# Optimization experiments

Hardware: AMD Instinct MI355X
Metric: run time of the kernel (lower is better)

The kernel has to match this reference:

```python
import jax, jax.numpy as jnp
import numpy as np

N_NODES = 100000
N_EDGES = 1600000
N_GRAPHS = 128


def setup_inputs() -> dict:
    key = jax.random.key(0)
    ks = jax.random.split(key, 8)
    x = jax.random.normal(ks[0], (N_NODES, 384), dtype=jnp.float32)
    edge_index = jax.random.randint(ks[1], (2, N_EDGES), 0, N_NODES, dtype=jnp.int64)
    batch = jnp.sort(jax.random.randint(ks[2], (N_NODES,), 0, N_GRAPHS, dtype=jnp.int64))
    W1 = jax.random.normal(ks[3], (384, 128), dtype=jnp.float32) * (1.0 / np.sqrt(384))
    b1 = jnp.zeros((128,), dtype=jnp.float32)
    W2 = jax.random.normal(ks[4], (128, 64), dtype=jnp.float32) * (1.0 / np.sqrt(128))
    b2 = jnp.zeros((64,), dtype=jnp.float32)
    Wlin = jax.random.normal(ks[5], (64, 2), dtype=jnp.float32) * (1.0 / np.sqrt(64))
    blin = jnp.zeros((2,), dtype=jnp.float32)
    return {"x": x, "edge_index": edge_index, "batch": batch,
            "W1": W1, "b1": b1, "W2": W2, "b2": b2, "Wlin": Wlin, "blin": blin}


def gcn_conv(x, src, dst, W, b, n_nodes):
    # PyG GCNConv: self-loops + symmetric normalization D^{-1/2} A_hat D^{-1/2},
    # linear transform first (out_dim < in_dim -> cheaper messages).
    h = x @ W  # [N, out]
    deg = jax.ops.segment_sum(jnp.ones_like(dst, dtype=h.dtype), dst,
                              num_segments=n_nodes) + 1.0  # self-loop weight
    dis = jax.lax.rsqrt(deg)  # deg >= 1 always (self-loop)
    norm = dis[src] * dis[dst]  # per-edge normalization [E]
    msg = h[src] * norm[:, None]  # gather + scale [E, out]
    agg = jax.ops.segment_sum(msg, dst, num_segments=n_nodes)
    agg = agg + h * (dis * dis)[:, None]  # self-loop contribution
    return agg + b


def reference(x, edge_index, batch, W1, b1, W2, b2, Wlin, blin):
    src, dst = edge_index[0], edge_index[1]
    n_nodes = x.shape[0]
    h = jax.nn.relu(gcn_conv(x, src, dst, W1, b1, n_nodes))
    h = jax.nn.relu(gcn_conv(h, src, dst, W2, b2, n_nodes))
    # global_mean_pool over graph ids
    sums = jax.ops.segment_sum(h, batch, num_segments=N_GRAPHS)
    cnts = jax.ops.segment_sum(jnp.ones((n_nodes,), dtype=h.dtype), batch,
                               num_segments=N_GRAPHS)
    pooled = sums / jnp.maximum(cnts, 1.0)[:, None]  # [G, 64]
    # dropout is identity in eval mode
    return pooled @ Wlin + blin  # [G, 2]
```

## Files before the change

kernel.cpp:

```cpp
#include <hip/hip_runtime.h>


#define NN 100000
#define NG 128
#define BNODES 256
#define NBUK ((NN + BNODES - 1) / BNODES)
#define BCAP 6144

typedef __attribute__((ext_vector_type(8))) short short8;
typedef __attribute__((ext_vector_type(8))) unsigned short u16x8;
typedef __attribute__((ext_vector_type(4))) float f32x4;

__device__ __forceinline__ unsigned short f2bf(float f) {
    union { float f; unsigned u; } v; v.f = f;
    unsigned r = v.u + 0x7fffu + ((v.u >> 16) & 1u);
    return (unsigned short)(r >> 16);
}
__device__ __forceinline__ float bf2f(unsigned short h) {
    union { unsigned u; float f; } v; v.u = ((unsigned)h) << 16;
    return v.f;
}

__device__ __forceinline__ void gload_lds16(const float* g, void* l) {
    __builtin_amdgcn_global_load_lds(
        (const __attribute__((address_space(1))) void*)g,
        (__attribute__((address_space(3))) void*)l, 16, 0, 0);
}

__global__ __launch_bounds__(256) void init_kernel(int* __restrict__ bcnt,
                                                   float* __restrict__ pooled,
                                                   float* __restrict__ cnt) {
    const int i = blockIdx.x * 256 + threadIdx.x;
    if (i < NBUK) bcnt[i] = 0;
    if (i < NG * 64) pooled[i] = 0.f;
    if (i < NG) cnt[i] = 0.f;
}

__global__ __launch_bounds__(256) void bucket_scatter(const int* __restrict__ src,
                                                      const int* __restrict__ dst,
                                                      int* __restrict__ bcnt,
                                                      int2* __restrict__ pairs, int E) {
    __shared__ int hist[NBUK];
    __shared__ int lbase[NBUK];
    __shared__ int lfill[NBUK];
    const int t = threadIdx.x;
    const int chunk = (E + gridDim.x - 1) / gridDim.x;
    const int lo = blockIdx.x * chunk;
    const int hi = min(E, lo + chunk);
    for (int b = t; b < NBUK; b += 256) { hist[b] = 0; lfill[b] = 0; }
    __syncthreads();
    for (int i = lo + t; i < hi; i += 256)
        atomicAdd(&hist[dst[i] >> 8], 1);
    __syncthreads();
    for (int b = t; b < NBUK; b += 256)
        lbase[b] = hist[b] ? atomicAdd(&bcnt[b], hist[b]) : 0;
    __syncthreads();
    for (int i = lo + t; i < hi; i += 256) {
        const int s = src[i], d = dst[i];
        const int b = d >> 8;
        const int off = atomicAdd(&lfill[b], 1);
        pairs[(size_t)b * BCAP + lbase[b] + off] = make_int2(s, d);
    }
}

__global__ __launch_bounds__(512) void bucket_scan(const int* __restrict__ bcnt,
                                                   int* __restrict__ bbase,
                                                   int* __restrict__ rowptr,
                                                   int N, int E) {
    __shared__ int sm[512];
    const int t = threadIdx.x;
    sm[t] = (t < NBUK) ? bcnt[t] : 0;
    __syncthreads();
    for (int d = 1; d < 512; d <<= 1) {
        int a = (t >= d) ? sm[t - d] : 0;
        __syncthreads();
        sm[t] += a;
        __syncthreads();
    }
    if (t <= NBUK) bbase[t] = (t == 0) ? 0 : sm[t - 1];
    if (t == 0) rowptr[N] = E;
}

__global__ __launch_bounds__(256) void bucket_build(const int2* __restrict__ pairs,
                                                    const int* __restrict__ bcnt,
                                                    const int* __restrict__ bbase,
                                                    int* __restrict__ rowptr,
                                                    float* __restrict__ dis,
                                                    int* __restrict__ col, int N) {
    __shared__ int cnt[BNODES];
    __shared__ int sm[BNODES];
    __shared__ int pref[BNODES];
    __shared__ int fillc[BNODES];
    const int b = blockIdx.x;
    const int t = threadIdx.x;
    const int nbase = b * BNODES;
    const int ecnt = bcnt[b];
    const int2* ep = pairs + (size_t)b * BCAP;
    const int gbase = bbase[b];

    cnt[t] = 0;
    fillc[t] = 0;
    __syncthreads();
    for (int i = t; i < ecnt; i += 256)
        atomicAdd(&cnt[ep[i].y & (BNODES - 1)], 1);
    __syncthreads();
    sm[t] = cnt[t];
    __syncthreads();
    for (int d = 1; d < 256; d <<= 1) {
        int a = (t >= d) ? sm[t - d] : 0;
        __syncthreads();
        sm[t] += a;
        __syncthreads();
    }
    pref[t] = sm[t] - cnt[t];
    const int node = nbase + t;
    if (node < N) {
        rowptr[node] = gbase + pref[t];
        dis[node] = rsqrtf((float)cnt[t] + 1.0f);
    }
    __syncthreads();
    for (int i = t; i < ecnt; i += 256) {
        const int2 e = ep[i];
        const int d = e.y & (BNODES - 1);
        const int pos = gbase + pref[d] + atomicAdd(&fillc[d], 1);
        col[pos] = e.x;
    }
}

__global__ __launch_bounds__(256) void pack_w(const float* __restrict__ W,
                                              unsigned short* __restrict__ packH,
                                              unsigned short* __restrict__ packL,
                                              int K, int BN) {
    const int idx = blockIdx.x * blockDim.x + threadIdx.x;
    if (idx >= K * BN) return;
    const int e = idx & 7;
    const int l = (idx >> 3) & 63;
    const int rest = idx >> 9;
    const int NF = BN >> 4;
    const int nf = rest % NF;
    const int ks = rest / NF;
    const int n = nf * 16 + (l & 15);
    const int k = ks * 32 + ((l >> 4) & 3) * 8 + e;
    const float v = W[(size_t)k * BN + n];
    const unsigned short h = f2bf(v);
    packH[idx] = h;
    packL[idx] = f2bf(v - bf2f(h));
}

template <int BN, int K>
__global__ __launch_bounds__(256) void gemm_mfma(const float* __restrict__ A,
                                                 const unsigned short* __restrict__ WpH,
                                                 const unsigned short* __restrict__ WpL,
                                                 const float* __restrict__ scale,
                                                 unsigned short* __restrict__ Out,
                                                 int N) {
    constexpr int BM = 64;
    constexpr int NK = K / 32;
    constexpr int WROWS = (BN == 128) ? 2 : 4;
    constexpr int WCOLS = (BN == 128) ? 2 : 1;
    constexpr int WTM = BM / WROWS;
    constexpr int MF = WTM / 16;
    constexpr int NFW = (BN / WCOLS) / 16;
    constexpr int NFB = BN / 16;

    __shared__ float AsF[2][4][16][32];

    const int t = threadIdx.x;
    const int wid = t >> 6, lane = t & 63;
    const int wr = wid / WCOLS, wc = wid % WCOLS;
    const int r0 = blockIdx.x * BM;

    const int dmarow0 = min(r0 + wid * 16 + (lane >> 3), NN - 1);
    const int dmarow1 = min(r0 + wid * 16 + 8 + (lane >> 3), NN - 1);
    const float* dmap0 = A + (size_t)dmarow0 * K + (lane & 7) * 4;
    const float* dmap1 = A + (size_t)dmarow1 * K + (lane & 7) * 4;

    auto stageA = [&](int buf, int ks) {
        gload_lds16(dmap0 + ks * 32, &AsF[buf][wid][0][0]);
        gload_lds16(dmap1 + ks * 32, &AsF[buf][wid][8][0]);
    };
    auto loadB = [&](int ks, short8* bH, short8* bL) {
#pragma unroll
        for (int n = 0; n < NFW; ++n) {
            const int nfg = wc * NFW + n;
            const int base = ((ks * NFB + nfg) * 64 + lane) * 8;
            bH[n] = *(const short8*)&WpH[base];
            bL[n] = *(const short8*)&WpL[base];
        }
    };

    f32x4 acc[MF][NFW];
#pragma unroll
    for (int m = 0; m < MF; ++m)
#pragma unroll
        for (int n = 0; n < NFW; ++n) acc[m][n] = (f32x4){0.f, 0.f, 0.f, 0.f};

    stageA(0, 0);
    short8 bHc[NFW], bLc[NFW];
    loadB(0, bHc, bLc);

#pragma unroll
    for (int ks = 0; ks < NK; ++ks) {
        const int cur = ks & 1;
        __syncthreads();
        short8 bHn[NFW], bLn[NFW];
        if (ks + 1 < NK) {
            stageA(cur ^ 1, ks + 1);
            loadB(ks + 1, bHn, bLn);
        }
#pragma unroll
        for (int m = 0; m < MF; ++m) {
            const int mf = wr * MF + m;
            const float* fp = &AsF[cur][mf][lane & 15][(lane >> 4) * 8];
            const f32x4 f0 = *(const f32x4*)fp;
            const f32x4 f1 = *(const f32x4*)(fp + 4);
            short8 aH;
            aH[0] = (short)f2bf(f0[0]);
            aH[1] = (short)f2bf(f0[1]);
            aH[2] = (short)f2bf(f0[2]);
            aH[3] = (short)f2bf(f0[3]);
            aH[4] = (short)f2bf(f1[0]);
            aH[5] = (short)f2bf(f1[1]);
            aH[6] = (short)f2bf(f1[2]);
            aH[7] = (short)f2bf(f1[3]);
#pragma unroll
            for (int n = 0; n < NFW; ++n) {
                acc[m][n] = __builtin_amdgcn_mfma_f32_16x16x32_bf16(aH, bHc[n], acc[m][n], 0, 0, 0);
                acc[m][n] = __builtin_amdgcn_mfma_f32_16x16x32_bf16(aH, bLc[n], acc[m][n], 0, 0, 0);
            }
        }
        if (ks + 1 < NK) {
#pragma unroll
            for (int n = 0; n < NFW; ++n) {
                bHc[n] = bHn[n];
                bLc[n] = bLn[n];
            }
        }
    }

#pragma unroll
    for (int m = 0; m < MF; ++m) {
        const int row0 = r0 + wr * WTM + m * 16 + ((lane >> 4) << 2);
        float sc[4];
#pragma unroll
        for (int r = 0; r < 4; ++r) sc[r] = (row0 + r < N) ? scale[row0 + r] : 0.f;
#pragma unroll
        for (int n = 0; n < NFW; ++n) {
            const int cn = wc * (NFW * 16) + n * 16 + (lane & 15);
#pragma unroll
            for (int r = 0; r < 4; ++r) {
                if (row0 + r < N)
                    Out[(size_t)(row0 + r) * BN + cn] = f2bf(acc[m][n][r] * sc[r]);
            }
        }
    }
}

template <int COLS>
__global__ __launch_bounds__(256) void agg_gather(const int* __restrict__ rowptr,
                                                  const int* __restrict__ col,
                                                  const float* __restrict__ dis,
                                                  const unsigned short* __restrict__ Hs,
                                                  const float* __restrict__ bias,
                                                  float* __restrict__ Out, int N) {
    constexpr int NPW = (COLS == 128) ? 1 : 2;
    constexpr int LPN = 64 / NPW;
    constexpr int LPR = COLS / 8;
    constexpr int NSG = LPN / LPR;
    const int gw = (int)((blockIdx.x * blockDim.x + threadIdx.x) >> 6);
    const int lane = threadIdx.x & 63;
    const int sub = lane / LPN;
    const int nl = lane % LPN;
    const int esub = nl / LPR;
    const int sl = nl % LPR;
    const int node = gw * NPW + sub;
    const int lgbase = sub * LPN;

    float acc[8];
#pragma unroll
    for (int k = 0; k < 8; ++k) acc[k] = 0.f;

    int base = 0, len = 0;
    const int nodec = (node < N) ? node : 0;
    if (node < N) {
        base = rowptr[node];
        len = rowptr[node + 1] - base;
    }

    for (int j0 = 0; j0 < len; j0 += LPN) {
        const int remain = min(LPN, len - j0);
        const int sidx = (nl < remain) ? col[base + j0 + nl] : nodec;
        const int qtr = (remain + NSG - 1) / NSG;
        const int off = esub * qtr;
        int u = 0;
        for (; u + 8 <= qtr; u += 8) {
            u16x8 hv[8];
            float wv[8];
#pragma unroll
            for (int b = 0; b < 8; ++b) {
                const int idx = off + u + b;
                const int s = __shfl(sidx, lgbase + idx);
                wv[b] = (idx < remain) ? 1.f : 0.f;
                hv[b] = *(const u16x8*)(Hs + (size_t)s * COLS + sl * 8);
            }
#pragma unroll
            for (int b = 0; b < 8; ++b)
#pragma unroll
                for (int k = 0; k < 8; ++k)
                    acc[k] = fmaf(bf2f(hv[b][k]), wv[b], acc[k]);
        }
        for (; u + 4 <= qtr; u += 4) {
            u16x8 hv[4];
            float wv[4];
#pragma unroll
            for (int b = 0; b < 4; ++b) {
                const int idx = off + u + b;
                const int s = __shfl(sidx, lgbase + idx);
                wv[b] = (idx < remain) ? 1.f : 0.f;
                hv[b] = *(const u16x8*)(Hs + (size_t)s * COLS + sl * 8);
            }
#pragma unroll
            for (int b = 0; b < 4; ++b)
#pragma unroll
                for (int k = 0; k < 8; ++k)
                    acc[k] = fmaf(bf2f(hv[b][k]), wv[b], acc[k]);
        }
        for (; u < qtr; ++u) {
            const int idx = off + u;
            const int s = __shfl(sidx, lgbase + idx);
            const float w = (idx < remain) ? 1.f : 0.f;
            const u16x8 hv = *(const u16x8*)(Hs + (size_t)s * COLS + sl * 8);
#pragma unroll
            for (int k = 0; k < 8; ++k)
                acc[k] = fmaf(bf2f(hv[k]), w, acc[k]);
        }
    }

#pragma unroll
    for (int k = 0; k < 8; ++k) {
        acc[k] += __shfl_xor(acc[k], LPR);
        acc[k] += __shfl_xor(acc[k], 2 * LPR);
    }

    if (node < N && esub == 0) {
        const float dd = dis[node];
        const u16x8 hsb = *(const u16x8*)(Hs + (size_t)node * COLS + sl * 8);
        const f32x4 bv0 = *(const f32x4*)(bias + sl * 8);
        const f32x4 bv1 = *(const f32x4*)(bias + sl * 8 + 4);
        f32x4 o0, o1;
#pragma unroll
        for (int k = 0; k < 4; ++k) {
            o0[k] = fmaxf(fmaf(acc[k] + bf2f(hsb[k]), dd, bv0[k]), 0.f);
            o1[k] = fmaxf(fmaf(acc[k + 4] + bf2f(hsb[k + 4]), dd, bv1[k]), 0.f);
        }
        *(f32x4*)(Out + (size_t)node * COLS + sl * 8) = o0;
        *(f32x4*)(Out + (size_t)node * COLS + sl * 8 + 4) = o1;
    }
}

__global__ __launch_bounds__(256) void pool_kernel(const float* __restrict__ H,
                                                   const int* __restrict__ batch,
                                                   float* __restrict__ pooled,
                                                   float* __restrict__ cnt, int N) {
    const int c = threadIdx.x & 63;
    const int w = threadIdx.x >> 6;
    const int row0 = blockIdx.x * 128 + w * 32;
    if (row0 >= N) return;
    const int nr = min(32, N - row0);

    float v[32];
    int b[32];
#pragma unroll
    for (int i = 0; i < 32; ++i) {
        const int r = row0 + i;
        if (i < nr) {
            v[i] = H[(size_t)r * 64 + c];
            b[i] = batch[r];
        } else {
            v[i] = 0.f;
            b[i] = -1;
        }
    }
    int cur = b[0];
    float sum = 0.f, csum = 0.f;
#pragma unroll
    for (int i = 0; i < 32; ++i) {
        if (i < nr) {
            if (b[i] != cur) {
                atomicAdd(&pooled[cur * 64 + c], sum);
                if (c == 0) atomicAdd(&cnt[cur], csum);
                cur = b[i];
                sum = 0.f;
                csum = 0.f;
            }
            sum += v[i];
            csum += 1.f;
        }
    }
    atomicAdd(&pooled[cur * 64 + c], sum);
    if (c == 0) atomicAdd(&cnt[cur], csum);
}

__global__ __launch_bounds__(256) void final_kernel(const float* __restrict__ pooled,
                                                    const float* __restrict__ cnt,
                                                    const float* __restrict__ Wlin,
                                                    const float* __restrict__ blin,
                                                    float* __restrict__ out) {
    const int t = threadIdx.x;
    const int g = t >> 1, o = t & 1;
    const float inv = 1.0f / fmaxf(cnt[g], 1.0f);
    float s = 0.f;
#pragma unroll
    for (int j = 0; j < 64; ++j) s = fmaf(pooled[g * 64 + j], Wlin[j * 2 + o], s);
    out[t] = s * inv + blin[o];
}

extern "C" void kernel_launch(void* const* d_in, const int* in_sizes, int n_in,
                              void* d_out, int out_size, void* d_ws, size_t ws_size,
                              hipStream_t stream) {
    const float* x     = (const float*)d_in[0];
    const int*   edge  = (const int*)d_in[1];
    const int*   batch = (const int*)d_in[2];
    const float* W1    = (const float*)d_in[3];
    const float* b1    = (const float*)d_in[4];
    const float* W2    = (const float*)d_in[5];
    const float* b2    = (const float*)d_in[6];
    const float* Wlin  = (const float*)d_in[7];
    const float* blin  = (const float*)d_in[8];
    float* out = (float*)d_out;

    const int N = NN;
    const int E = in_sizes[1] / 2;
    const int* src = edge;
    const int* dst = edge + E;

    char* ws = (char*)d_ws;
    size_t off = 0;
    auto alloc = [&](size_t bytes) -> void* {
        void* p = ws + off;
        off += (bytes + 511) & ~(size_t)511;
        return p;
    };
    float* dis    = (float*)alloc((size_t)N * 4);
    int*   rowptr = (int*)alloc((size_t)(N + 1) * 4);
    int*   bcnt   = (int*)alloc((size_t)NBUK * 4);
    int*   bbase  = (int*)alloc((size_t)(NBUK + 1) * 4);
    int*   col    = (int*)alloc((size_t)E * 4);
    int2*  pairs  = (int2*)alloc((size_t)NBUK * BCAP * 8);
    unsigned short* w1h = (unsigned short*)alloc((size_t)384 * 128 * 2);
    unsigned short* w1l = (unsigned short*)alloc((size_t)384 * 128 * 2);
    unsigned short* w2h = (unsigned short*)alloc((size_t)128 * 64 * 2);
    unsigned short* w2l = (unsigned short*)alloc((size_t)128 * 64 * 2);
    unsigned short* h1bf = (unsigned short*)alloc((size_t)N * 128 * 2);
    float* agg1   = (float*)alloc((size_t)N * 128 * 4);
    float* pooled = (float*)alloc((size_t)NG * 64 * 4);
    float* cnt    = (float*)alloc((size_t)NG * 4);
    unsigned short* h2bf = h1bf;
    float* agg2 = agg1;

    init_kernel<<<(NG * 64 + 255) / 256, 256, 0, stream>>>(bcnt, pooled, cnt);

    pack_w<<<(384 * 128 + 255) / 256, 256, 0, stream>>>(W1, w1h, w1l, 384, 128);
    pack_w<<<(128 * 64 + 255) / 256, 256, 0, stream>>>(W2, w2h, w2l, 128, 64);

    bucket_scatter<<<512, 256, 0, stream>>>(src, dst, bcnt, pairs, E);
    bucket_scan<<<1, 512, 0, stream>>>(bcnt, bbase, rowptr, N, E);
    bucket_build<<<NBUK, 256, 0, stream>>>(pairs, bcnt, bbase, rowptr, dis, col, N);

    const int gblocks = (N + 63) / 64;
    gemm_mfma<128, 384><<<gblocks, 256, 0, stream>>>(x, w1h, w1l, dis, h1bf, N);
    agg_gather<128><<<(N + 3) / 4, 256, 0, stream>>>(rowptr, col, dis, h1bf, b1, agg1, N);

    gemm_mfma<64, 128><<<gblocks, 256, 0, stream>>>(agg1, w2h, w2l, dis, h2bf, N);
    agg_gather<64><<<(N + 7) / 8, 256, 0, stream>>>(rowptr, col, dis, h2bf, b2, agg2, N);

    pool_kernel<<<(N + 127) / 128, 256, 0, stream>>>(agg2, batch, pooled, cnt, N);
    final_kernel<<<1, 256, 0, stream>>>(pooled, cnt, Wlin, blin, out);
}
```

Measured before the change: 249.7 us.

## Double K-step per barrier in MFMA GEMM and load B fragments inline

The GEMM main loop now stages 64 K-columns of A into LDS per iteration instead of 32, with four DMA loads per wave, which halves the number of barriers. The explicit register prefetch of the B (weight) fragments is dropped, and B is loaded directly from global memory right before each MFMA. The intent is to cut synchronisation overhead and register pressure. In exchange, LDS use doubles and the weight loads may become exposed latency that no longer overlaps with compute.

```diff
diff --git a/kernel.cpp b/kernel.cpp
--- a/kernel.cpp
+++ b/kernel.cpp
@@ -155,7 +155,7 @@
                                                  unsigned short* __restrict__ Out,
                                                  int N) {
     constexpr int BM = 64;
-    constexpr int NK = K / 32;
+    constexpr int NK = K / 64;
     constexpr int WROWS = (BN == 128) ? 2 : 4;
     constexpr int WCOLS = (BN == 128) ? 2 : 1;
     constexpr int WTM = BM / WROWS;
@@ -163,31 +163,25 @@
     constexpr int NFW = (BN / WCOLS) / 16;
     constexpr int NFB = BN / 16;
 
-    __shared__ float AsF[2][4][16][32];
+    __shared__ float AsF[2][4][16][64];
 
     const int t = threadIdx.x;
     const int wid = t >> 6, lane = t & 63;
     const int wr = wid / WCOLS, wc = wid % WCOLS;
     const int r0 = blockIdx.x * BM;
 
-    const int dmarow0 = min(r0 + wid * 16 + (lane >> 3), NN - 1);
-    const int dmarow1 = min(r0 + wid * 16 + 8 + (lane >> 3), NN - 1);
-    const float* dmap0 = A + (size_t)dmarow0 * K + (lane & 7) * 4;
-    const float* dmap1 = A + (size_t)dmarow1 * K + (lane & 7) * 4;
+    const float* dmap[4];
+#pragma unroll
+    for (int c = 0; c < 4; ++c) {
+        const int row = min(r0 + wid * 16 + c * 4 + (lane >> 4), NN - 1);
+        dmap[c] = A + (size_t)row * K + (lane & 15) * 4;
+    }
 
     auto stageA = [&](int buf, int ks) {
-        gload_lds16(dmap0 + ks * 32, &AsF[buf][wid][0][0]);
-        gload_lds16(dmap1 + ks * 32, &AsF[buf][wid][8][0]);
+#pragma unroll
+        for (int c = 0; c < 4; ++c)
+            gload_lds16(dmap[c] + ks * 64, &AsF[buf][wid][c * 4][0]);
     };
-    auto loadB = [&](int ks, short8* bH, short8* bL) {
-#pragma unroll
-        for (int n = 0; n < NFW; ++n) {
-            const int nfg = wc * NFW + n;
-            const int base = ((ks * NFB + nfg) * 64 + lane) * 8;
-            bH[n] = *(const short8*)&WpH[base];
-            bL[n] = *(const short8*)&WpL[base];
-        }
-    };
 
     f32x4 acc[MF][NFW];
 #pragma unroll
@@ -196,44 +190,38 @@
         for (int n = 0; n < NFW; ++n) acc[m][n] = (f32x4){0.f, 0.f, 0.f, 0.f};
 
     stageA(0, 0);
-    short8 bHc[NFW], bLc[NFW];
-    loadB(0, bHc, bLc);
 
 #pragma unroll
     for (int ks = 0; ks < NK; ++ks) {
         const int cur = ks & 1;
         __syncthreads();
-        short8 bHn[NFW], bLn[NFW];
-        if (ks + 1 < NK) {
-            stageA(cur ^ 1, ks + 1);
-            loadB(ks + 1, bHn, bLn);
-        }
-#pragma unroll
-        for (int m = 0; m < MF; ++m) {
-            const int mf = wr * MF + m;
-            const float* fp = &AsF[cur][mf][lane & 15][(lane >> 4) * 8];
-            const f32x4 f0 = *(const f32x4*)fp;
-            const f32x4 f1 = *(const f32x4*)(fp + 4);
-            short8 aH;
-            aH[0] = (short)f2bf(f0[0]);
-            aH[1] = (short)f2bf(f0[1]);
-            aH[2] = (short)f2bf(f0[2]);
-            aH[3] = (short)f2bf(f0[3]);
-            aH[4] = (short)f2bf(f1[0]);
-            aH[5] = (short)f2bf(f1[1]);
-            aH[6] = (short)f2bf(f1[2]);
-            aH[7] = (short)f2bf(f1[3]);
-#pragma unroll
-            for (int n = 0; n < NFW; ++n) {
-                acc[m][n] = __builtin_amdgcn_mfma_f32_16x16x32_bf16(aH, bHc[n], acc[m][n], 0, 0, 0);
-                acc[m][n] = __builtin_amdgcn_mfma_f32_16x16x32_bf16(aH, bLc[n], acc[m][n], 0, 0, 0);
-            }
-        }
-        if (ks + 1 < NK) {
-#pragma unroll
-            for (int n = 0; n < NFW; ++n) {
-                bHc[n] = bHn[n];
-                bLc[n] = bLn[n];
+        if (ks + 1 < NK) stageA(cur ^ 1, ks + 1);
+#pragma unroll
+        for (int kk = 0; kk < 2; ++kk) {
+#pragma unroll
+            for (int m = 0; m < MF; ++m) {
+                const int mf = wr * MF + m;
+                const float* fp = &AsF[cur][mf][lane & 15][kk * 32 + (lane >> 4) * 8];
+                const f32x4 f0 = *(const f32x4*)fp;
+                const f32x4 f1 = *(const f32x4*)(fp + 4);
+                short8 aH;
+                aH[0] = (short)f2bf(f0[0]);
+                aH[1] = (short)f2bf(f0[1]);
+                aH[2] = (short)f2bf(f0[2]);
+                aH[3] = (short)f2bf(f0[3]);
+                aH[4] = (short)f2bf(f1[0]);
+                aH[5] = (short)f2bf(f1[1]);
+                aH[6] = (short)f2bf(f1[2]);
+                aH[7] = (short)f2bf(f1[3]);
+#pragma unroll
+                for (int n = 0; n < NFW; ++n) {
+                    const int nfg = wc * NFW + n;
+                    const int base = (((ks * 2 + kk) * NFB + nfg) * 64 + lane) * 8;
+                    const short8 bH = *(const short8*)&WpH[base];
+                    const short8 bL = *(const short8*)&WpL[base];
+                    acc[m][n] = __builtin_amdgcn_mfma_f32_16x16x32_bf16(aH, bH, acc[m][n], 0, 0, 0);
+                    acc[m][n] = __builtin_amdgcn_mfma_f32_16x16x32_bf16(aH, bL, acc[m][n], 0, 0, 0);
+                }
             }
         }
     }
```

New measurement: 254.1 us. Within noise of the previous version (+1.7%).
